# Kernel tuning notes

Measured on AMD Instinct MI355X. Metric: run time of the kernel, lower is better.

Reference implementation:

```python
import jax, jax.numpy as jnp
import numpy as np

N = 50000   # nodes
E = 1600000 # edges (avg degree 32)
H = 128     # input_size == hidden_size
L = 2       # n_layer


def setup_inputs() -> dict:
    key = jax.random.key(0)
    k0, k1, k2, k3, k4 = jax.random.split(key, 5)
    inp = jax.random.normal(k0, (N, H), dtype=jnp.float32)
    h = jax.random.normal(k1, (L, N, H), dtype=jnp.float32)
    edgidx = jax.random.randint(k2, (2, E), 0, N, dtype=jnp.int32)
    # stacked gate linears, order per layer: xz, hz, xr, hr, xh, hh
    W = jax.random.normal(k3, (L, 6, H, H), dtype=jnp.float32) * (1.0 / np.sqrt(H))
    b = jax.random.normal(k4, (L, 6, H), dtype=jnp.float32) * 0.01
    return {"inp": inp, "edgidx": edgidx, "h": h, "W": W, "b": b}


def _gin(x, W, b, src, dst, n):
    # GINConv with eps=0: Linear(x + sum_{j in N(i)} x_j)
    agg = jax.ops.segment_sum(x[src], dst, num_segments=n)  # scatter-add over edges
    return (x + agg) @ W + b


def reference(inp, edgidx, h, W, b):
    src, dst = edgidx[0], edgidx[1]
    n = inp.shape[0]
    x = inp
    outs = []
    for i in range(W.shape[0]):  # small fixed layer loop
        z = jax.nn.sigmoid(_gin(x, W[i, 0], b[i, 0], src, dst, n)
                           + _gin(h[i], W[i, 1], b[i, 1], src, dst, n))
        r = jax.nn.sigmoid(_gin(x, W[i, 2], b[i, 2], src, dst, n)
                           + _gin(h[i], W[i, 3], b[i, 3], src, dst, n))
        h_tilde = jnp.tanh(_gin(x, W[i, 4], b[i, 4], src, dst, n)
                           + _gin(r * h[i], W[i, 5], b[i, 5], src, dst, n))
        x = z * h[i] + (1.0 - z) * h_tilde
        outs.append(x)
    h_out = jnp.stack(outs)  # [L, N, H]; original returns (out, h_out) where out is h_out
    return h_out
```

## Files before the change

### kernel.cpp

```cpp
#include <hip/hip_runtime.h>
#include <math.h>
#include <stdint.h>

#define HDIM 128

typedef _Float16 f16;
typedef unsigned short u16;
typedef __attribute__((ext_vector_type(8))) unsigned short u16x8;
typedef __attribute__((ext_vector_type(4))) _Float16 f16x4;
typedef __attribute__((ext_vector_type(8))) _Float16 f16x8;
typedef __attribute__((ext_vector_type(4))) float f32x4;

__global__ __launch_bounds__(256) void degrank_kernel(
    const int* __restrict__ edg, int* __restrict__ cnt,
    u16* __restrict__ rank, int E) {
  int e = blockIdx.x * 256 + threadIdx.x;
  if (e < E) {
    int src = edg[e];
    int dst = edg[E + e];
    rank[e] = (u16)atomicAdd(&cnt[dst * 16 + (src >> 12)], 1);
  }
}

__global__ __launch_bounds__(256) void nodescan_kernel(
    int* __restrict__ cnt, int* __restrict__ deg, int* __restrict__ degt,
    int N) {
  int node = blockIdx.x * 256 + threadIdx.x;
  if (node >= N) return;
  int* c = cnt + node * 16;
  int s = 0;
  #pragma unroll
  for (int b = 0; b < 16; ++b) {
    int v = c[b];
    c[b] = s;
    s += v;
  }
  degt[node] = s;
  deg[node] = (s + 7) & ~7;
}

__global__ __launch_bounds__(256) void scan_part_kernel(
    const int* __restrict__ deg, int* __restrict__ bsum, int n, int chunk) {
  __shared__ int red[256];
  const int b = blockIdx.x, t = threadIdx.x;
  const int begin = b * chunk;
  const int end = min(begin + chunk, n);
  int s = 0;
  for (int i = begin + t; i < end; i += 256) s += deg[i];
  red[t] = s;
  __syncthreads();
  for (int off = 128; off > 0; off >>= 1) {
    if (t < off) red[t] += red[t + off];
    __syncthreads();
  }
  if (t == 0) bsum[b] = red[0];
}

__global__ __launch_bounds__(256) void scan_top_kernel(
    const int* __restrict__ bsum, int* __restrict__ boff,
    int* __restrict__ offs, int n) {
  __shared__ int sh[256];
  const int t = threadIdx.x;
  int v = bsum[t];
  sh[t] = v;
  __syncthreads();
  for (int off = 1; off < 256; off <<= 1) {
    int add = (t >= off) ? sh[t - off] : 0;
    __syncthreads();
    sh[t] += add;
    __syncthreads();
  }
  boff[t] = sh[t] - v;
  if (t == 255) offs[n] = sh[255];
}

__global__ __launch_bounds__(256) void scan_fin_kernel(
    const int* __restrict__ deg, const int* __restrict__ boff,
    int* __restrict__ offs, int n, int chunk) {
  __shared__ int sh[256];
  const int b = blockIdx.x, t = threadIdx.x;
  const int idx = b * chunk + t;
  int v = (t < chunk && idx < n) ? deg[idx] : 0;
  sh[t] = v;
  __syncthreads();
  for (int off = 1; off < 256; off <<= 1) {
    int add = (t >= off) ? sh[t - off] : 0;
    __syncthreads();
    sh[t] += add;
    __syncthreads();
  }
  if (t < chunk && idx < n) offs[idx] = boff[b] + sh[t] - v;
}

__global__ __launch_bounds__(256) void fill_kernel(
    const int* __restrict__ edg, const int* __restrict__ offs,
    const int* __restrict__ cnt, const u16* __restrict__ rank,
    u16* __restrict__ csr_src, int E) {
  int i = blockIdx.x * 256 + threadIdx.x;
  int e0 = i * 4;
  if (e0 >= E) return;
  if (e0 + 4 <= E) {
    int4 s4 = *reinterpret_cast<const int4*>(edg + e0);
    int4 d4 = *reinterpret_cast<const int4*>(edg + E + e0);
    ushort4 r4 = *reinterpret_cast<const ushort4*>(rank + e0);
    csr_src[offs[d4.x] + cnt[d4.x * 16 + (s4.x >> 12)] + r4.x] = (u16)s4.x;
    csr_src[offs[d4.y] + cnt[d4.y * 16 + (s4.y >> 12)] + r4.y] = (u16)s4.y;
    csr_src[offs[d4.z] + cnt[d4.z * 16 + (s4.z >> 12)] + r4.z] = (u16)s4.z;
    csr_src[offs[d4.w] + cnt[d4.w * 16 + (s4.w >> 12)] + r4.w] = (u16)s4.w;
  } else {
    for (int e = e0; e < E; ++e) {
      int src = edg[e];
      int dst = edg[E + e];
      csr_src[offs[dst] + cnt[dst * 16 + (src >> 12)] + rank[e]] = (u16)src;
    }
  }
}

__global__ __launch_bounds__(256) void pad_kernel(
    const int* __restrict__ offs, const int* __restrict__ degt,
    const int* __restrict__ deg, u16* __restrict__ csr,
    f16* __restrict__ xb, f16* __restrict__ Pb, f16* __restrict__ hb,
    int N, int L) {
  int n = blockIdx.x * 256 + threadIdx.x;
  if (n < N) {
    int base = offs[n];
    int a = degt[n], b = deg[n];
    for (int k = base + a; k < base + b; ++k) csr[k] = (u16)N;
  } else {
    int t2 = n - N;
    int rows = 2 + L;
    int total = 4 * rows * 4;
    if (t2 < total) {
      int chunk = t2 & 3;
      int r = (t2 >> 2) % rows;
      int sl = (t2 >> 2) / rows;
      size_t SN1 = (size_t)(N + 1);
      f16* p;
      if (r == 0)      p = xb + (sl * SN1 + N) * 32;
      else if (r == 1) p = Pb + (sl * SN1 + N) * 32;
      else {
        int i = r - 2;
        p = hb + ((size_t)sl * L * SN1 + (size_t)i * SN1 + N) * 32;
      }
      f16x8 z{};
      *reinterpret_cast<f16x8*>(p + chunk * 8) = z;
    }
  }
}

__global__ __launch_bounds__(256) void convb_kernel(
    const float* __restrict__ inp, const float* __restrict__ h,
    f16* __restrict__ xb, f16* __restrict__ hb, int n, int N1, int NH,
    int L) {
  const int ly = blockIdx.y;
  const float* __restrict__ src = (ly == 0) ? inp : h + (size_t)(ly - 1) * NH;
  f16* __restrict__ dstb = (ly == 0) ? xb : hb;
  const int SN = (ly == 0) ? N1 : L * N1;
  const int rowoff = (ly == 0) ? 0 : (ly - 1) * N1;
  const int t = threadIdx.x;
  const int nloc = t >> 3;
  const int sub = t & 7;
  const int sl = sub >> 1;
  const int hf = sub & 1;
  const int node = blockIdx.x * 32 + nloc;
  if (node >= n) return;
  const float* sp = src + (size_t)node * HDIM + sub * 16;
  f16* dp = dstb + ((size_t)sl * SN + rowoff + node) * 32 + hf * 16;
  float4 v0 = *reinterpret_cast<const float4*>(sp + 0);
  float4 v1 = *reinterpret_cast<const float4*>(sp + 4);
  float4 v2 = *reinterpret_cast<const float4*>(sp + 8);
  float4 v3 = *reinterpret_cast<const float4*>(sp + 12);
  f16x8 o0, o1;
  o0[0]=(f16)v0.x; o0[1]=(f16)v0.y; o0[2]=(f16)v0.z; o0[3]=(f16)v0.w;
  o0[4]=(f16)v1.x; o0[5]=(f16)v1.y; o0[6]=(f16)v1.z; o0[7]=(f16)v1.w;
  o1[0]=(f16)v2.x; o1[1]=(f16)v2.y; o1[2]=(f16)v2.z; o1[3]=(f16)v2.w;
  o1[4]=(f16)v3.x; o1[5]=(f16)v3.y; o1[6]=(f16)v3.z; o1[7]=(f16)v3.w;
  *reinterpret_cast<f16x8*>(dp) = o0;
  *reinterpret_cast<f16x8*>(dp + 8) = o1;
}

__global__ __launch_bounds__(256) void transw_kernel(
    const float* __restrict__ W, f16* __restrict__ WT) {
  __shared__ float sh[32][33];
  const int g = blockIdx.y;
  const int ti = blockIdx.x >> 2;
  const int tj = blockIdx.x & 3;
  const float* __restrict__ wp = W + (size_t)g * HDIM * HDIM;
  f16* __restrict__ op = WT + (size_t)g * HDIM * HDIM;
  const int t = threadIdx.x;
  #pragma unroll
  for (int it = 0; it < 4; ++it) {
    int elem = it * 256 + t;
    int r = elem >> 5, c = elem & 31;
    sh[r][c] = wp[(size_t)(ti * 32 + r) * HDIM + tj * 32 + c];
  }
  __syncthreads();
  #pragma unroll
  for (int it = 0; it < 4; ++it) {
    int elem = it * 256 + t;
    int cc = elem >> 5, rr = elem & 31;
    op[(size_t)(tj * 32 + cc) * HDIM + ti * 32 + rr] = (f16)sh[rr][cc];
  }
}

__global__ __launch_bounds__(256) void pull2_kernel(
    const u16* __restrict__ csr_src, const int* __restrict__ offs,
    const f16* __restrict__ xb, const f16* __restrict__ hbl,
    f16* __restrict__ A, f16* __restrict__ Bh, int N, int N1, int hSN) {
  const int cls = blockIdx.x & 7;
  const int tid = cls >> 2;
  const int sl = cls & 3;
  const int node = (blockIdx.x >> 3) * 64 + (threadIdx.x >> 2);
  if (node >= N) return;
  const int c8 = (threadIdx.x & 3) << 3;
  const f16* __restrict__ tab =
      tid ? hbl + (size_t)sl * hSN * 32 : xb + (size_t)sl * (size_t)N1 * 32;
  f16* __restrict__ dst = (tid ? Bh : A) + (size_t)sl * (size_t)N1 * 32;
  const int s = offs[node];
  const int e = offs[node + 1];
  float acc[8];
  f16x8 sv = *reinterpret_cast<const f16x8*>(tab + (size_t)node * 32 + c8);
  #pragma unroll
  for (int q = 0; q < 8; ++q) acc[q] = (float)sv[q];
  int k = s;
  for (; k + 16 <= e; k += 16) {
    u16x8 ia = *reinterpret_cast<const u16x8*>(csr_src + k);
    u16x8 ib = *reinterpret_cast<const u16x8*>(csr_src + k + 8);
    f16x8 u0 = *reinterpret_cast<const f16x8*>(tab + (size_t)ia[0] * 32 + c8);
    f16x8 u1 = *reinterpret_cast<const f16x8*>(tab + (size_t)ia[1] * 32 + c8);
    f16x8 u2 = *reinterpret_cast<const f16x8*>(tab + (size_t)ia[2] * 32 + c8);
    f16x8 u3 = *reinterpret_cast<const f16x8*>(tab + (size_t)ia[3] * 32 + c8);
    f16x8 u4 = *reinterpret_cast<const f16x8*>(tab + (size_t)ia[4] * 32 + c8);
    f16x8 u5 = *reinterpret_cast<const f16x8*>(tab + (size_t)ia[5] * 32 + c8);
    f16x8 u6 = *reinterpret_cast<const f16x8*>(tab + (size_t)ia[6] * 32 + c8);
    f16x8 u7 = *reinterpret_cast<const f16x8*>(tab + (size_t)ia[7] * 32 + c8);
    f16x8 u8 = *reinterpret_cast<const f16x8*>(tab + (size_t)ib[0] * 32 + c8);
    f16x8 u9 = *reinterpret_cast<const f16x8*>(tab + (size_t)ib[1] * 32 + c8);
    f16x8 ua = *reinterpret_cast<const f16x8*>(tab + (size_t)ib[2] * 32 + c8);
    f16x8 ub = *reinterpret_cast<const f16x8*>(tab + (size_t)ib[3] * 32 + c8);
    f16x8 uc = *reinterpret_cast<const f16x8*>(tab + (size_t)ib[4] * 32 + c8);
    f16x8 ud = *reinterpret_cast<const f16x8*>(tab + (size_t)ib[5] * 32 + c8);
    f16x8 ue = *reinterpret_cast<const f16x8*>(tab + (size_t)ib[6] * 32 + c8);
    f16x8 uf = *reinterpret_cast<const f16x8*>(tab + (size_t)ib[7] * 32 + c8);
    f16x8 g0 = (u0 + u1) + (u2 + u3);
    f16x8 g1 = (u4 + u5) + (u6 + u7);
    f16x8 g2 = (u8 + u9) + (ua + ub);
    f16x8 g3 = (uc + ud) + (ue + uf);
    #pragma unroll
    for (int q = 0; q < 8; ++q)
      acc[q] += ((float)g0[q] + (float)g1[q]) + ((float)g2[q] + (float)g3[q]);
  }
  if (k < e) {
    u16x8 ia = *reinterpret_cast<const u16x8*>(csr_src + k);
    f16x8 u0 = *reinterpret_cast<const f16x8*>(tab + (size_t)ia[0] * 32 + c8);
    f16x8 u1 = *reinterpret_cast<const f16x8*>(tab + (size_t)ia[1] * 32 + c8);
    f16x8 u2 = *reinterpret_cast<const f16x8*>(tab + (size_t)ia[2] * 32 + c8);
    f16x8 u3 = *reinterpret_cast<const f16x8*>(tab + (size_t)ia[3] * 32 + c8);
    f16x8 u4 = *reinterpret_cast<const f16x8*>(tab + (size_t)ia[4] * 32 + c8);
    f16x8 u5 = *reinterpret_cast<const f16x8*>(tab + (size_t)ia[5] * 32 + c8);
    f16x8 u6 = *reinterpret_cast<const f16x8*>(tab + (size_t)ia[6] * 32 + c8);
    f16x8 u7 = *reinterpret_cast<const f16x8*>(tab + (size_t)ia[7] * 32 + c8);
    f16x8 g0 = (u0 + u1) + (u2 + u3);
    f16x8 g1 = (u4 + u5) + (u6 + u7);
    #pragma unroll
    for (int q = 0; q < 8; ++q) acc[q] += (float)g0[q] + (float)g1[q];
  }
  f16x8 o;
  #pragma unroll
  for (int q = 0; q < 8; ++q) o[q] = (f16)acc[q];
  *reinterpret_cast<f16x8*>(dst + (size_t)node * 32 + c8) = o;
}

__device__ __forceinline__ void stage_blocked(
    const f16* __restrict__ src, f16* __restrict__ As,
    int row0, int N, int SN, int t) {
  #pragma unroll
  for (int i = 0; i < 4; ++i) {
    int u = i * 256 + t;
    int row = u >> 4;
    int sl = (u >> 2) & 3;
    int ck = u & 3;
    int r = row0 + row;
    f16x8 v{};
    if (r < N) v = *reinterpret_cast<const f16x8*>(
        src + ((size_t)sl * SN + r) * 32 + ck * 8);
    *reinterpret_cast<f16x8*>(&As[row * 136 + sl * 32 + ck * 8]) = v;
  }
}

__device__ __forceinline__ void mfma_tile(
    const f16* As, const f16* Ws, int wr, int wc, int ln15, int quad,
    f32x4 (&acc)[2][4]) {
  #pragma unroll
  for (int s = 0; s < 4; ++s) {
    f16x8 a0 = *reinterpret_cast<const f16x8*>(
        &As[(wr * 32 + ln15) * 136 + s * 32 + quad * 8]);
    f16x8 a1 = *reinterpret_cast<const f16x8*>(
        &As[(wr * 32 + 16 + ln15) * 136 + s * 32 + quad * 8]);
    #pragma unroll
    for (int ni = 0; ni < 4; ++ni) {
      f16x8 bf = *reinterpret_cast<const f16x8*>(
          &Ws[(wc * 64 + ni * 16 + ln15) * 136 + s * 32 + quad * 8]);
      acc[0][ni] = __builtin_amdgcn_mfma_f32_16x16x32_f16(a0, bf, acc[0][ni], 0, 0, 0);
      acc[1][ni] = __builtin_amdgcn_mfma_f32_16x16x32_f16(a1, bf, acc[1][ni], 0, 0, 0);
    }
  }
}

__global__ __launch_bounds__(256, 3) void gemm3_kernel(
    const f16* __restrict__ A, const f16* __restrict__ Bh,
    const f16* __restrict__ WT, const float* __restrict__ b,
    const f16* __restrict__ hbl, f16* __restrict__ zb,
    f16* __restrict__ P, float* __restrict__ hpre, int N, int N1, int hSN) {
  __shared__ f16 As[64 * 136];
  __shared__ f16 Ws[128 * 136];
  const int t = threadIdx.x;
  const int w = t >> 6, wr = w >> 1, wc = w & 1;
  const int lane = t & 63, ln15 = lane & 15, quad = lane >> 4;
  const int row0 = blockIdx.x * 64;
  f32x4 accZ[2][4], accR[2][4], accH[2][4];
  #pragma unroll
  for (int i = 0; i < 2; ++i)
    #pragma unroll
    for (int j = 0; j < 4; ++j) {
      accZ[i][j] = (f32x4){0.f, 0.f, 0.f, 0.f};
      accR[i][j] = (f32x4){0.f, 0.f, 0.f, 0.f};
      accH[i][j] = (f32x4){0.f, 0.f, 0.f, 0.f};
    }

  stage_blocked(A, As, row0, N, N1, t);
  #pragma unroll
  for (int g = 0; g < 3; ++g) {
    const f16* __restrict__ wp = WT + (size_t)(g * 2) * HDIM * HDIM;
    __syncthreads();
    #pragma unroll
    for (int i = 0; i < 8; ++i) {
      int flat = i * 256 + t;
      int n = flat >> 4;
      int o = (flat & 15) * 8;
      *reinterpret_cast<f16x8*>(&Ws[n * 136 + o]) =
          *reinterpret_cast<const f16x8*>(wp + (size_t)n * HDIM + o);
    }
    __syncthreads();
    if (g == 0) mfma_tile(As, Ws, wr, wc, ln15, quad, accZ);
    else if (g == 1) mfma_tile(As, Ws, wr, wc, ln15, quad, accR);
    else mfma_tile(As, Ws, wr, wc, ln15, quad, accH);
  }
  __syncthreads();
  stage_blocked(Bh, As, row0, N, N1, t);
  #pragma unroll
  for (int g = 0; g < 2; ++g) {
    const f16* __restrict__ wp = WT + (size_t)(g * 2 + 1) * HDIM * HDIM;
    __syncthreads();
    #pragma unroll
    for (int i = 0; i < 8; ++i) {
      int flat = i * 256 + t;
      int n = flat >> 4;
      int o = (flat & 15) * 8;
      *reinterpret_cast<f16x8*>(&Ws[n * 136 + o]) =
          *reinterpret_cast<const f16x8*>(wp + (size_t)n * HDIM + o);
    }
    __syncthreads();
    if (g == 0) mfma_tile(As, Ws, wr, wc, ln15, quad, accZ);
    else mfma_tile(As, Ws, wr, wc, ln15, quad, accR);
  }
  __syncthreads();

  {
    const f16* __restrict__ wp = WT + (size_t)5 * HDIM * HDIM;
    #pragma unroll
    for (int i = 0; i < 8; ++i) {
      int flat = i * 256 + t;
      int n = flat >> 4;
      int o = (flat & 15) * 8;
      *reinterpret_cast<f16x8*>(&Ws[n * 136 + o]) =
          *reinterpret_cast<const f16x8*>(wp + (size_t)n * HDIM + o);
    }
  }
  #pragma unroll
  for (int ni = 0; ni < 4; ++ni) {
    const int col = wc * 64 + ni * 16 + ln15;
    const int slc = col >> 5;
    const int cw = col & 31;
    float bz = b[0 * HDIM + col] + b[1 * HDIM + col];
    float br = b[2 * HDIM + col] + b[3 * HDIM + col];
    float bh = b[4 * HDIM + col] + b[5 * HDIM + col];
    #pragma unroll
    for (int mi = 0; mi < 2; ++mi) {
      #pragma unroll
      for (int r = 0; r < 4; ++r) {
        int rowl = wr * 32 + mi * 16 + quad * 4 + r;
        int row = row0 + rowl;
        float rv = accR[mi][ni][r] + br;
        float rg = 1.f / (1.f + expf(-rv));
        float hv = 0.f;
        if (row < N) {
          size_t idx = (size_t)row * HDIM + col;
          zb[idx] = (f16)(accZ[mi][ni][r] + bz);
          hpre[idx] = accH[mi][ni][r] + bh;
          hv = (float)hbl[((size_t)slc * hSN + row) * 32 + cw];
        }
        As[rowl * 136 + col] = (f16)(rg * hv);
      }
    }
  }
  __syncthreads();
  f32x4 accP[2][4];
  #pragma unroll
  for (int i = 0; i < 2; ++i)
    #pragma unroll
    for (int j = 0; j < 4; ++j) accP[i][j] = (f32x4){0.f, 0.f, 0.f, 0.f};
  mfma_tile(As, Ws, wr, wc, ln15, quad, accP);

  #pragma unroll
  for (int ni = 0; ni < 4; ++ni) {
    const int col = wc * 64 + ni * 16 + ln15;
    const int slc = col >> 5;
    const int cw = col & 31;
    #pragma unroll
    for (int mi = 0; mi < 2; ++mi) {
      #pragma unroll
      for (int r = 0; r < 4; ++r) {
        int row = row0 + wr * 32 + mi * 16 + quad * 4 + r;
        if (row >= N) continue;
        P[((size_t)slc * N1 + row) * 32 + cw] = (f16)accP[mi][ni][r];
      }
    }
  }
}

__global__ __launch_bounds__(256) void gru_final_kernel(
    const u16* __restrict__ csr_src, const int* __restrict__ offs,
    const f16* __restrict__ P, const f16* __restrict__ zb,
    const f16* __restrict__ hbl, float* __restrict__ outi,
    f16* __restrict__ xb, int N, int N1, int hSN) {
  const int sl = blockIdx.x & 3;
  const int node = (blockIdx.x >> 2) * 64 + (threadIdx.x >> 2);
  if (node >= N) return;
  const int c8 = (threadIdx.x & 3) << 3;
  const f16* __restrict__ tab = P + (size_t)sl * (size_t)N1 * 32;
  const int s = offs[node];
  const int e = offs[node + 1];
  float acc[8];
  f16x8 sv = *reinterpret_cast<const f16x8*>(tab + (size_t)node * 32 + c8);
  #pragma unroll
  for (int q = 0; q < 8; ++q) acc[q] = (float)sv[q];
  int k = s;
  for (; k + 16 <= e; k += 16) {
    u16x8 ia = *reinterpret_cast<const u16x8*>(csr_src + k);
    u16x8 ib = *reinterpret_cast<const u16x8*>(csr_src + k + 8);
    f16x8 u0 = *reinterpret_cast<const f16x8*>(tab + (size_t)ia[0] * 32 + c8);
    f16x8 u1 = *reinterpret_cast<const f16x8*>(tab + (size_t)ia[1] * 32 + c8);
    f16x8 u2 = *reinterpret_cast<const f16x8*>(tab + (size_t)ia[2] * 32 + c8);
    f16x8 u3 = *reinterpret_cast<const f16x8*>(tab + (size_t)ia[3] * 32 + c8);
    f16x8 u4 = *reinterpret_cast<const f16x8*>(tab + (size_t)ia[4] * 32 + c8);
    f16x8 u5 = *reinterpret_cast<const f16x8*>(tab + (size_t)ia[5] * 32 + c8);
    f16x8 u6 = *reinterpret_cast<const f16x8*>(tab + (size_t)ia[6] * 32 + c8);
    f16x8 u7 = *reinterpret_cast<const f16x8*>(tab + (size_t)ia[7] * 32 + c8);
    f16x8 u8 = *reinterpret_cast<const f16x8*>(tab + (size_t)ib[0] * 32 + c8);
    f16x8 u9 = *reinterpret_cast<const f16x8*>(tab + (size_t)ib[1] * 32 + c8);
    f16x8 ua = *reinterpret_cast<const f16x8*>(tab + (size_t)ib[2] * 32 + c8);
    f16x8 ub = *reinterpret_cast<const f16x8*>(tab + (size_t)ib[3] * 32 + c8);
    f16x8 uc = *reinterpret_cast<const f16x8*>(tab + (size_t)ib[4] * 32 + c8);
    f16x8 ud = *reinterpret_cast<const f16x8*>(tab + (size_t)ib[5] * 32 + c8);
    f16x8 ue = *reinterpret_cast<const f16x8*>(tab + (size_t)ib[6] * 32 + c8);
    f16x8 uf = *reinterpret_cast<const f16x8*>(tab + (size_t)ib[7] * 32 + c8);
    f16x8 g0 = (u0 + u1) + (u2 + u3);
    f16x8 g1 = (u4 + u5) + (u6 + u7);
    f16x8 g2 = (u8 + u9) + (ua + ub);
    f16x8 g3 = (uc + ud) + (ue + uf);
    #pragma unroll
    for (int q = 0; q < 8; ++q)
      acc[q] += ((float)g0[q] + (float)g1[q]) + ((float)g2[q] + (float)g3[q]);
  }
  if (k < e) {
    u16x8 ia = *reinterpret_cast<const u16x8*>(csr_src + k);
    f16x8 u0 = *reinterpret_cast<const f16x8*>(tab + (size_t)ia[0] * 32 + c8);
    f16x8 u1 = *reinterpret_cast<const f16x8*>(tab + (size_t)ia[1] * 32 + c8);
    f16x8 u2 = *reinterpret_cast<const f16x8*>(tab + (size_t)ia[2] * 32 + c8);
    f16x8 u3 = *reinterpret_cast<const f16x8*>(tab + (size_t)ia[3] * 32 + c8);
    f16x8 u4 = *reinterpret_cast<const f16x8*>(tab + (size_t)ia[4] * 32 + c8);
    f16x8 u5 = *reinterpret_cast<const f16x8*>(tab + (size_t)ia[5] * 32 + c8);
    f16x8 u6 = *reinterpret_cast<const f16x8*>(tab + (size_t)ia[6] * 32 + c8);
    f16x8 u7 = *reinterpret_cast<const f16x8*>(tab + (size_t)ia[7] * 32 + c8);
    f16x8 g0 = (u0 + u1) + (u2 + u3);
    f16x8 g1 = (u4 + u5) + (u6 + u7);
    #pragma unroll
    for (int q = 0; q < 8; ++q) acc[q] += (float)g0[q] + (float)g1[q];
  }
  const size_t idx = (size_t)node * HDIM + sl * 32 + c8;
  float4 hp0 = *reinterpret_cast<const float4*>(outi + idx);
  float4 hp1 = *reinterpret_cast<const float4*>(outi + idx + 4);
  f16x8 zv = *reinterpret_cast<const f16x8*>(zb + idx);
  f16x8 hv = *reinterpret_cast<const f16x8*>(
      hbl + ((size_t)sl * hSN + node) * 32 + c8);
  float4 o0, o1;
  f16x8 xo;
  #pragma unroll
  for (int q = 0; q < 8; ++q) {
    float hp = (q < 4) ? (&hp0.x)[q] : (&hp1.x)[q - 4];
    float ht = tanhf(hp + acc[q]);
    float z = 1.f / (1.f + expf(-(float)zv[q]));
    float o = z * (float)hv[q] + (1.f - z) * ht;
    if (q < 4) (&o0.x)[q] = o; else (&o1.x)[q - 4] = o;
    xo[q] = (f16)o;
  }
  *reinterpret_cast<float4*>(outi + idx) = o0;
  *reinterpret_cast<float4*>(outi + idx + 4) = o1;
  *reinterpret_cast<f16x8*>(xb + ((size_t)sl * N1 + node) * 32 + c8) = xo;
}

extern "C" void kernel_launch(void* const* d_in, const int* in_sizes, int n_in,
                              void* d_out, int out_size, void* d_ws, size_t ws_size,
                              hipStream_t stream) {
  const float* inp = (const float*)d_in[0];
  const int*   edg = (const int*)d_in[1];
  const float* h   = (const float*)d_in[2];
  const float* W   = (const float*)d_in[3];
  const float* b   = (const float*)d_in[4];
  float* out = (float*)d_out;

  const int NH = in_sizes[0];
  const int N  = NH / HDIM;
  const int E  = in_sizes[1] / 2;
  const int L  = in_sizes[2] / NH;
  const int N1 = N + 1;
  const size_t NT = (size_t)128 * N1;

  f16* Af   = (f16*)d_ws;
  f16* Bhf  = Af + NT;
  f16* Pbuf = Bhf + NT;
  f16* xbuf = Pbuf + NT;
  f16* hbuf = xbuf + NT;
  f16* zbuf = hbuf + (size_t)L * NT;
  f16* WT   = zbuf + (size_t)NH;
  int* deg     = (int*)(WT + (size_t)L * 6 * HDIM * HDIM);
  int* degt    = deg + N;
  int* offs    = degt + N;
  int* bsum    = offs + (N + 1);
  int* boff    = bsum + 256;
  uintptr_t rp = (uintptr_t)(boff + 256);
  rp = (rp + 63) & ~(uintptr_t)63;
  u16* rank    = (u16*)rp;
  u16* csr_src = rank + (size_t)E;
  int* cnt     = (int*)Af;

  const int eblocks = (E + 255) / 256;
  const int fblocks = (E + 1023) / 1024;
  const int nsblocks = (N + 255) / 256;
  const int pdblocks = (N + 256 + 255) / 256;
  const int rowblocks = (N + 63) / 64;
  const int p2blocks = ((N + 63) / 64) * 8;
  const int p1blocks = ((N + 63) / 64) * 4;
  const int cvblocks = (N + 31) / 32;
  const int chunk = (N + 255) / 256;
  const int hSN = L * N1;

  hipMemsetAsync(cnt, 0, (size_t)N * 16 * sizeof(int), stream);
  hipLaunchKernelGGL(degrank_kernel, dim3(eblocks), dim3(256), 0, stream,
                     edg, cnt, rank, E);
  hipLaunchKernelGGL(nodescan_kernel, dim3(nsblocks), dim3(256), 0, stream,
                     cnt, deg, degt, N);
  hipLaunchKernelGGL(scan_part_kernel, dim3(256), dim3(256), 0, stream,
                     deg, bsum, N, chunk);
  hipLaunchKernelGGL(scan_top_kernel, dim3(1), dim3(256), 0, stream,
                     bsum, boff, offs, N);
  hipLaunchKernelGGL(scan_fin_kernel, dim3(256), dim3(256), 0, stream,
                     deg, boff, offs, N, chunk);
  hipLaunchKernelGGL(fill_kernel, dim3(fblocks), dim3(256), 0, stream,
                     edg, offs, cnt, rank, csr_src, E);
  hipLaunchKernelGGL(pad_kernel, dim3(pdblocks), dim3(256), 0, stream,
                     offs, degt, deg, csr_src, xbuf, Pbuf, hbuf, N, L);
  hipLaunchKernelGGL(transw_kernel, dim3(16, L * 6), dim3(256), 0, stream,
                     W, WT);
  hipLaunchKernelGGL(convb_kernel, dim3(cvblocks, L + 1), dim3(256), 0, stream,
                     inp, h, xbuf, hbuf, N, N1, NH, L);

  for (int i = 0; i < L; ++i) {
    const f16* hbl = hbuf + (size_t)i * N1 * 32;
    const f16* WTi = WT + (size_t)i * 6 * HDIM * HDIM;
    const float* bi = b + (size_t)i * 6 * HDIM;
    float* outi = out + (size_t)i * NH;

    hipLaunchKernelGGL(pull2_kernel, dim3(p2blocks), dim3(256), 0, stream,
                       csr_src, offs, xbuf, hbl, Af, Bhf, N, N1, hSN);
    hipLaunchKernelGGL(gemm3_kernel, dim3(rowblocks), dim3(256), 0, stream,
                       Af, Bhf, WTi, bi, hbl, zbuf, Pbuf, outi, N, N1, hSN);
    hipLaunchKernelGGL(gru_final_kernel, dim3(p1blocks), dim3(256), 0, stream,
                       csr_src, offs, Pbuf, zbuf, hbl, outi, xbuf, N, N1, hSN);
  }
}
```

Measured before the change: 591.7 us.

## Fuse preprocessing kernels and overlap next-layer h aggregation with GRU final

Merges the node scan with the block partial sum, and merges the three-stage scan into a two-kernel scan. It also fuses the CSR fill with the padding, and the weight transpose with the fp16 conversion, to cut launch count. The h[i+1] neighbour aggregation moves into the previous layer's gru_final launch as extra block classes, so the later layer only pulls x. This removes several small launches and fills the GPU better during the final gather. In exchange it adds divergent block roles and a single-block-level scan over bsum in every scanfin block.

```diff
diff --git a/kernel.cpp b/kernel.cpp
--- a/kernel.cpp
+++ b/kernel.cpp
@@ -22,46 +22,42 @@
   }
 }
 
-__global__ __launch_bounds__(256) void nodescan_kernel(
+__global__ __launch_bounds__(256) void nodescan2_kernel(
     int* __restrict__ cnt, int* __restrict__ deg, int* __restrict__ degt,
-    int N) {
-  int node = blockIdx.x * 256 + threadIdx.x;
-  if (node >= N) return;
-  int* c = cnt + node * 16;
-  int s = 0;
-  #pragma unroll
-  for (int b = 0; b < 16; ++b) {
-    int v = c[b];
-    c[b] = s;
-    s += v;
-  }
-  degt[node] = s;
-  deg[node] = (s + 7) & ~7;
-}
-
-__global__ __launch_bounds__(256) void scan_part_kernel(
-    const int* __restrict__ deg, int* __restrict__ bsum, int n, int chunk) {
+    int* __restrict__ bsum, int N) {
   __shared__ int red[256];
-  const int b = blockIdx.x, t = threadIdx.x;
-  const int begin = b * chunk;
-  const int end = min(begin + chunk, n);
-  int s = 0;
-  for (int i = begin + t; i < end; i += 256) s += deg[i];
-  red[t] = s;
+  const int t = threadIdx.x;
+  const int node = blockIdx.x * 256 + t;
+  int d8 = 0;
+  if (node < N) {
+    int* c = cnt + node * 16;
+    int s = 0;
+    #pragma unroll
+    for (int b2 = 0; b2 < 16; ++b2) {
+      int v = c[b2];
+      c[b2] = s;
+      s += v;
+    }
+    degt[node] = s;
+    d8 = (s + 7) & ~7;
+    deg[node] = d8;
+  }
+  red[t] = d8;
   __syncthreads();
   for (int off = 128; off > 0; off >>= 1) {
     if (t < off) red[t] += red[t + off];
     __syncthreads();
   }
-  if (t == 0) bsum[b] = red[0];
-}
-
-__global__ __launch_bounds__(256) void scan_top_kernel(
-    const int* __restrict__ bsum, int* __restrict__ boff,
-    int* __restrict__ offs, int n) {
+  if (t == 0) bsum[blockIdx.x] = red[0];
+}
+
+__global__ __launch_bounds__(256) void scanfin2_kernel(
+    const int* __restrict__ deg, const int* __restrict__ bsum,
+    int* __restrict__ offs, int N, int nblk) {
   __shared__ int sh[256];
   const int t = threadIdx.x;
-  int v = bsum[t];
+  const int b = blockIdx.x;
+  int v = (t < nblk) ? bsum[t] : 0;
   sh[t] = v;
   __syncthreads();
   for (int off = 1; off < 256; off <<= 1) {
@@ -70,18 +66,11 @@
     sh[t] += add;
     __syncthreads();
   }
-  boff[t] = sh[t] - v;
-  if (t == 255) offs[n] = sh[255];
-}
-
-__global__ __launch_bounds__(256) void scan_fin_kernel(
-    const int* __restrict__ deg, const int* __restrict__ boff,
-    int* __restrict__ offs, int n, int chunk) {
-  __shared__ int sh[256];
-  const int b = blockIdx.x, t = threadIdx.x;
-  const int idx = b * chunk + t;
-  int v = (t < chunk && idx < n) ? deg[idx] : 0;
-  sh[t] = v;
+  const int boff = sh[b] - bsum[b];
+  __syncthreads();
+  const int idx = b * 256 + t;
+  int dv = (idx < N) ? deg[idx] : 0;
+  sh[t] = dv;
   __syncthreads();
   for (int off = 1; off < 256; off <<= 1) {
     int add = (t >= off) ? sh[t - off] : 0;
@@ -89,45 +78,43 @@
     sh[t] += add;
     __syncthreads();
   }
-  if (t < chunk && idx < n) offs[idx] = boff[b] + sh[t] - v;
-}
-
-__global__ __launch_bounds__(256) void fill_kernel(
+  if (idx < N) {
+    offs[idx] = boff + sh[t] - dv;
+    if (idx == N - 1) offs[N] = boff + sh[t];
+  }
+}
+
+__global__ __launch_bounds__(256) void fillpad_kernel(
     const int* __restrict__ edg, const int* __restrict__ offs,
     const int* __restrict__ cnt, const u16* __restrict__ rank,
-    u16* __restrict__ csr_src, int E) {
+    const int* __restrict__ degt, const int* __restrict__ deg,
+    u16* __restrict__ csr_src, f16* __restrict__ xb, f16* __restrict__ Pb,
+    f16* __restrict__ hb, int E, int N, int L) {
   int i = blockIdx.x * 256 + threadIdx.x;
   int e0 = i * 4;
-  if (e0 >= E) return;
-  if (e0 + 4 <= E) {
-    int4 s4 = *reinterpret_cast<const int4*>(edg + e0);
-    int4 d4 = *reinterpret_cast<const int4*>(edg + E + e0);
-    ushort4 r4 = *reinterpret_cast<const ushort4*>(rank + e0);
-    csr_src[offs[d4.x] + cnt[d4.x * 16 + (s4.x >> 12)] + r4.x] = (u16)s4.x;
-    csr_src[offs[d4.y] + cnt[d4.y * 16 + (s4.y >> 12)] + r4.y] = (u16)s4.y;
-    csr_src[offs[d4.z] + cnt[d4.z * 16 + (s4.z >> 12)] + r4.z] = (u16)s4.z;
-    csr_src[offs[d4.w] + cnt[d4.w * 16 + (s4.w >> 12)] + r4.w] = (u16)s4.w;
+  if (e0 < E) {
+    if (e0 + 4 <= E) {
+      int4 s4 = *reinterpret_cast<const int4*>(edg + e0);
+      int4 d4 = *reinterpret_cast<const int4*>(edg + E + e0);
+      ushort4 r4 = *reinterpret_cast<const ushort4*>(rank + e0);
+      csr_src[offs[d4.x] + cnt[d4.x * 16 + (s4.x >> 12)] + r4.x] = (u16)s4.x;
+      csr_src[offs[d4.y] + cnt[d4.y * 16 + (s4.y >> 12)] + r4.y] = (u16)s4.y;
+      csr_src[offs[d4.z] + cnt[d4.z * 16 + (s4.z >> 12)] + r4.z] = (u16)s4.z;
+      csr_src[offs[d4.w] + cnt[d4.w * 16 + (s4.w >> 12)] + r4.w] = (u16)s4.w;
+    } else {
+      for (int e = e0; e < E; ++e) {
+        int src = edg[e];
+        int dst = edg[E + e];
+        csr_src[offs[dst] + cnt[dst * 16 + (src >> 12)] + rank[e]] = (u16)src;
+      }
+    }
+  }
+  if (i < N) {
+    int base = offs[i];
+    int a = degt[i], b2 = deg[i];
+    for (int k = base + a; k < base + b2; ++k) csr_src[k] = (u16)N;
   } else {
-    for (int e = e0; e < E; ++e) {
-      int src = edg[e];
-      int dst = edg[E + e];
-      csr_src[offs[dst] + cnt[dst * 16 + (src >> 12)] + rank[e]] = (u16)src;
-    }
-  }
-}
-
-__global__ __launch_bounds__(256) void pad_kernel(
-    const int* __restrict__ offs, const int* __restrict__ degt,
-    const int* __restrict__ deg, u16* __restrict__ csr,
-    f16* __restrict__ xb, f16* __restrict__ Pb, f16* __restrict__ hb,
-    int N, int L) {
-  int n = blockIdx.x * 256 + threadIdx.x;
-  if (n < N) {
-    int base = offs[n];
-    int a = degt[n], b = deg[n];
-    for (int k = base + a; k < base + b; ++k) csr[k] = (u16)N;
-  } else {
-    int t2 = n - N;
+    int t2 = i - N;
     int rows = 2 + L;
     int total = 4 * rows * 4;
     if (t2 < total) {
@@ -139,8 +126,8 @@
       if (r == 0)      p = xb + (sl * SN1 + N) * 32;
       else if (r == 1) p = Pb + (sl * SN1 + N) * 32;
       else {
-        int i = r - 2;
-        p = hb + ((size_t)sl * L * SN1 + (size_t)i * SN1 + N) * 32;
+        int li = r - 2;
+        p = hb + ((size_t)sl * L * SN1 + (size_t)li * SN1 + N) * 32;
       }
       f16x8 z{};
       *reinterpret_cast<f16x8*>(p + chunk * 8) = z;
@@ -148,84 +135,68 @@
   }
 }
 
-__global__ __launch_bounds__(256) void convb_kernel(
+__global__ __launch_bounds__(256) void transconv_kernel(
     const float* __restrict__ inp, const float* __restrict__ h,
-    f16* __restrict__ xb, f16* __restrict__ hb, int n, int N1, int NH,
-    int L) {
+    const float* __restrict__ W, f16* __restrict__ xb, f16* __restrict__ hb,
+    f16* __restrict__ WT, int n, int N1, int NH, int L) {
+  __shared__ float shm[32][33];
   const int ly = blockIdx.y;
-  const float* __restrict__ src = (ly == 0) ? inp : h + (size_t)(ly - 1) * NH;
-  f16* __restrict__ dstb = (ly == 0) ? xb : hb;
-  const int SN = (ly == 0) ? N1 : L * N1;
-  const int rowoff = (ly == 0) ? 0 : (ly - 1) * N1;
   const int t = threadIdx.x;
-  const int nloc = t >> 3;
-  const int sub = t & 7;
-  const int sl = sub >> 1;
-  const int hf = sub & 1;
-  const int node = blockIdx.x * 32 + nloc;
-  if (node >= n) return;
-  const float* sp = src + (size_t)node * HDIM + sub * 16;
-  f16* dp = dstb + ((size_t)sl * SN + rowoff + node) * 32 + hf * 16;
-  float4 v0 = *reinterpret_cast<const float4*>(sp + 0);
-  float4 v1 = *reinterpret_cast<const float4*>(sp + 4);
-  float4 v2 = *reinterpret_cast<const float4*>(sp + 8);
-  float4 v3 = *reinterpret_cast<const float4*>(sp + 12);
-  f16x8 o0, o1;
-  o0[0]=(f16)v0.x; o0[1]=(f16)v0.y; o0[2]=(f16)v0.z; o0[3]=(f16)v0.w;
-  o0[4]=(f16)v1.x; o0[5]=(f16)v1.y; o0[6]=(f16)v1.z; o0[7]=(f16)v1.w;
-  o1[0]=(f16)v2.x; o1[1]=(f16)v2.y; o1[2]=(f16)v2.z; o1[3]=(f16)v2.w;
-  o1[4]=(f16)v3.x; o1[5]=(f16)v3.y; o1[6]=(f16)v3.z; o1[7]=(f16)v3.w;
-  *reinterpret_cast<f16x8*>(dp) = o0;
-  *reinterpret_cast<f16x8*>(dp + 8) = o1;
-}
-
-__global__ __launch_bounds__(256) void transw_kernel(
-    const float* __restrict__ W, f16* __restrict__ WT) {
-  __shared__ float sh[32][33];
-  const int g = blockIdx.y;
-  const int ti = blockIdx.x >> 2;
-  const int tj = blockIdx.x & 3;
-  const float* __restrict__ wp = W + (size_t)g * HDIM * HDIM;
-  f16* __restrict__ op = WT + (size_t)g * HDIM * HDIM;
-  const int t = threadIdx.x;
-  #pragma unroll
-  for (int it = 0; it < 4; ++it) {
-    int elem = it * 256 + t;
-    int r = elem >> 5, c = elem & 31;
-    sh[r][c] = wp[(size_t)(ti * 32 + r) * HDIM + tj * 32 + c];
-  }
-  __syncthreads();
-  #pragma unroll
-  for (int it = 0; it < 4; ++it) {
-    int elem = it * 256 + t;
-    int cc = elem >> 5, rr = elem & 31;
-    op[(size_t)(tj * 32 + cc) * HDIM + ti * 32 + rr] = (f16)sh[rr][cc];
-  }
-}
-
-__global__ __launch_bounds__(256) void pull2_kernel(
-    const u16* __restrict__ csr_src, const int* __restrict__ offs,
-    const f16* __restrict__ xb, const f16* __restrict__ hbl,
-    f16* __restrict__ A, f16* __restrict__ Bh, int N, int N1, int hSN) {
-  const int cls = blockIdx.x & 7;
-  const int tid = cls >> 2;
-  const int sl = cls & 3;
-  const int node = (blockIdx.x >> 3) * 64 + (threadIdx.x >> 2);
-  if (node >= N) return;
-  const int c8 = (threadIdx.x & 3) << 3;
-  const f16* __restrict__ tab =
-      tid ? hbl + (size_t)sl * hSN * 32 : xb + (size_t)sl * (size_t)N1 * 32;
-  f16* __restrict__ dst = (tid ? Bh : A) + (size_t)sl * (size_t)N1 * 32;
-  const int s = offs[node];
-  const int e = offs[node + 1];
-  float acc[8];
-  f16x8 sv = *reinterpret_cast<const f16x8*>(tab + (size_t)node * 32 + c8);
-  #pragma unroll
-  for (int q = 0; q < 8; ++q) acc[q] = (float)sv[q];
+  if (ly <= L) {
+    const float* __restrict__ src = (ly == 0) ? inp : h + (size_t)(ly - 1) * NH;
+    f16* __restrict__ dstb = (ly == 0) ? xb : hb;
+    const int SN = (ly == 0) ? N1 : L * N1;
+    const int rowoff = (ly == 0) ? 0 : (ly - 1) * N1;
+    const int nloc = t >> 3;
+    const int sub = t & 7;
+    const int sl = sub >> 1;
+    const int hf = sub & 1;
+    const int node = blockIdx.x * 32 + nloc;
+    if (node >= n) return;
+    const float* sp = src + (size_t)node * HDIM + sub * 16;
+    f16* dp = dstb + ((size_t)sl * SN + rowoff + node) * 32 + hf * 16;
+    float4 v0 = *reinterpret_cast<const float4*>(sp + 0);
+    float4 v1 = *reinterpret_cast<const float4*>(sp + 4);
+    float4 v2 = *reinterpret_cast<const float4*>(sp + 8);
+    float4 v3 = *reinterpret_cast<const float4*>(sp + 12);
+    f16x8 o0, o1;
+    o0[0]=(f16)v0.x; o0[1]=(f16)v0.y; o0[2]=(f16)v0.z; o0[3]=(f16)v0.w;
+    o0[4]=(f16)v1.x; o0[5]=(f16)v1.y; o0[6]=(f16)v1.z; o0[7]=(f16)v1.w;
+    o1[0]=(f16)v2.x; o1[1]=(f16)v2.y; o1[2]=(f16)v2.z; o1[3]=(f16)v2.w;
+    o1[4]=(f16)v3.x; o1[5]=(f16)v3.y; o1[6]=(f16)v3.z; o1[7]=(f16)v3.w;
+    *reinterpret_cast<f16x8*>(dp) = o0;
+    *reinterpret_cast<f16x8*>(dp + 8) = o1;
+  } else {
+    if (blockIdx.x >= 16 * L * 6) return;
+    const int g = blockIdx.x >> 4;
+    const int inner = blockIdx.x & 15;
+    const int ti = inner >> 2;
+    const int tj = inner & 3;
+    const float* __restrict__ wp = W + (size_t)g * HDIM * HDIM;
+    f16* __restrict__ op = WT + (size_t)g * HDIM * HDIM;
+    #pragma unroll
+    for (int it = 0; it < 4; ++it) {
+      int elem = it * 256 + t;
+      int r = elem >> 5, c = elem & 31;
+      shm[r][c] = wp[(size_t)(ti * 32 + r) * HDIM + tj * 32 + c];
+    }
+    __syncthreads();
+    #pragma unroll
+    for (int it = 0; it < 4; ++it) {
+      int elem = it * 256 + t;
+      int cc = elem >> 5, rr = elem & 31;
+      op[(size_t)(tj * 32 + cc) * HDIM + ti * 32 + rr] = (f16)shm[rr][cc];
+    }
+  }
+}
+
+__device__ __forceinline__ void gather8(
+    const u16* __restrict__ csr, int s, int e, const f16* __restrict__ tab,
+    int c8, float acc[8]) {
   int k = s;
   for (; k + 16 <= e; k += 16) {
-    u16x8 ia = *reinterpret_cast<const u16x8*>(csr_src + k);
-    u16x8 ib = *reinterpret_cast<const u16x8*>(csr_src + k + 8);
+    u16x8 ia = *reinterpret_cast<const u16x8*>(csr + k);
+    u16x8 ib = *reinterpret_cast<const u16x8*>(csr + k + 8);
     f16x8 u0 = *reinterpret_cast<const f16x8*>(tab + (size_t)ia[0] * 32 + c8);
     f16x8 u1 = *reinterpret_cast<const f16x8*>(tab + (size_t)ia[1] * 32 + c8);
     f16x8 u2 = *reinterpret_cast<const f16x8*>(tab + (size_t)ia[2] * 32 + c8);
@@ -251,7 +222,7 @@
       acc[q] += ((float)g0[q] + (float)g1[q]) + ((float)g2[q] + (float)g3[q]);
   }
   if (k < e) {
-    u16x8 ia = *reinterpret_cast<const u16x8*>(csr_src + k);
+    u16x8 ia = *reinterpret_cast<const u16x8*>(csr + k);
     f16x8 u0 = *reinterpret_cast<const f16x8*>(tab + (size_t)ia[0] * 32 + c8);
     f16x8 u1 = *reinterpret_cast<const f16x8*>(tab + (size_t)ia[1] * 32 + c8);
     f16x8 u2 = *reinterpret_cast<const f16x8*>(tab + (size_t)ia[2] * 32 + c8);
@@ -265,6 +236,46 @@
     #pragma unroll
     for (int q = 0; q < 8; ++q) acc[q] += (float)g0[q] + (float)g1[q];
   }
+}
+
+__global__ __launch_bounds__(256) void pull2_kernel(
+    const u16* __restrict__ csr_src, const int* __restrict__ offs,
+    const f16* __restrict__ xb, const f16* __restrict__ hbl,
+    f16* __restrict__ A, f16* __restrict__ Bh, int N, int N1, int hSN) {
+  const int cls = blockIdx.x & 7;
+  const int tid = cls >> 2;
+  const int sl = cls & 3;
+  const int node = (blockIdx.x >> 3) * 64 + (threadIdx.x >> 2);
+  if (node >= N) return;
+  const int c8 = (threadIdx.x & 3) << 3;
+  const f16* __restrict__ tab =
+      tid ? hbl + (size_t)sl * hSN * 32 : xb + (size_t)sl * (size_t)N1 * 32;
+  f16* __restrict__ dst = (tid ? Bh : A) + (size_t)sl * (size_t)N1 * 32;
+  float acc[8];
+  f16x8 sv = *reinterpret_cast<const f16x8*>(tab + (size_t)node * 32 + c8);
+  #pragma unroll
+  for (int q = 0; q < 8; ++q) acc[q] = (float)sv[q];
+  gather8(csr_src, offs[node], offs[node + 1], tab, c8, acc);
+  f16x8 o;
+  #pragma unroll
+  for (int q = 0; q < 8; ++q) o[q] = (f16)acc[q];
+  *reinterpret_cast<f16x8*>(dst + (size_t)node * 32 + c8) = o;
+}
+
+__global__ __launch_bounds__(256) void pullx_kernel(
+    const u16* __restrict__ csr_src, const int* __restrict__ offs,
+    const f16* __restrict__ tabb, f16* __restrict__ dstb, int N, int N1) {
+  const int sl = blockIdx.x & 3;
+  const int node = (blockIdx.x >> 2) * 64 + (threadIdx.x >> 2);
+  if (node >= N) return;
+  const int c8 = (threadIdx.x & 3) << 3;
+  const f16* __restrict__ tab = tabb + (size_t)sl * (size_t)N1 * 32;
+  f16* __restrict__ dst = dstb + (size_t)sl * (size_t)N1 * 32;
+  float acc[8];
+  f16x8 sv = *reinterpret_cast<const f16x8*>(tab + (size_t)node * 32 + c8);
+  #pragma unroll
+  for (int q = 0; q < 8; ++q) acc[q] = (float)sv[q];
+  gather8(csr_src, offs[node], offs[node + 1], tab, c8, acc);
   f16x8 o;
   #pragma unroll
   for (int q = 0; q < 8; ++q) o[q] = (f16)acc[q];
@@ -433,61 +444,34 @@
     const u16* __restrict__ csr_src, const int* __restrict__ offs,
     const f16* __restrict__ P, const f16* __restrict__ zb,
     const f16* __restrict__ hbl, float* __restrict__ outi,
-    f16* __restrict__ xb, int N, int N1, int hSN) {
-  const int sl = blockIdx.x & 3;
-  const int node = (blockIdx.x >> 2) * 64 + (threadIdx.x >> 2);
+    f16* __restrict__ xb, const f16* __restrict__ hnext,
+    f16* __restrict__ Bh, int N, int N1, int hSN, int lgc) {
+  const int cls = blockIdx.x & ((1 << lgc) - 1);
+  const int node = (blockIdx.x >> lgc) * 64 + (threadIdx.x >> 2);
   if (node >= N) return;
   const int c8 = (threadIdx.x & 3) << 3;
+  if (cls >= 4) {
+    const int sl = cls - 4;
+    const f16* __restrict__ tab = hnext + (size_t)sl * hSN * 32;
+    f16* __restrict__ dst = Bh + (size_t)sl * (size_t)N1 * 32;
+    float acc[8];
+    f16x8 sv = *reinterpret_cast<const f16x8*>(tab + (size_t)node * 32 + c8);
+    #pragma unroll
+    for (int q = 0; q < 8; ++q) acc[q] = (float)sv[q];
+    gather8(csr_src, offs[node], offs[node + 1], tab, c8, acc);
+    f16x8 o;
+    #pragma unroll
+    for (int q = 0; q < 8; ++q) o[q] = (f16)acc[q];
+    *reinterpret_cast<f16x8*>(dst + (size_t)node * 32 + c8) = o;
+    return;
+  }
+  const int sl = cls;
   const f16* __restrict__ tab = P + (size_t)sl * (size_t)N1 * 32;
-  const int s = offs[node];
-  const int e = offs[node + 1];
   float acc[8];
   f16x8 sv = *reinterpret_cast<const f16x8*>(tab + (size_t)node * 32 + c8);
   #pragma unroll
   for (int q = 0; q < 8; ++q) acc[q] = (float)sv[q];
-  int k = s;
-  for (; k + 16 <= e; k += 16) {
-    u16x8 ia = *reinterpret_cast<const u16x8*>(csr_src + k);
-    u16x8 ib = *reinterpret_cast<const u16x8*>(csr_src + k + 8);
-    f16x8 u0 = *reinterpret_cast<const f16x8*>(tab + (size_t)ia[0] * 32 + c8);
-    f16x8 u1 = *reinterpret_cast<const f16x8*>(tab + (size_t)ia[1] * 32 + c8);
-    f16x8 u2 = *reinterpret_cast<const f16x8*>(tab + (size_t)ia[2] * 32 + c8);
-    f16x8 u3 = *reinterpret_cast<const f16x8*>(tab + (size_t)ia[3] * 32 + c8);
-    f16x8 u4 = *reinterpret_cast<const f16x8*>(tab + (size_t)ia[4] * 32 + c8);
-    f16x8 u5 = *reinterpret_cast<const f16x8*>(tab + (size_t)ia[5] * 32 + c8);
-    f16x8 u6 = *reinterpret_cast<const f16x8*>(tab + (size_t)ia[6] * 32 + c8);
-    f16x8 u7 = *reinterpret_cast<const f16x8*>(tab + (size_t)ia[7] * 32 + c8);
-    f16x8 u8 = *reinterpret_cast<const f16x8*>(tab + (size_t)ib[0] * 32 + c8);
-    f16x8 u9 = *reinterpret_cast<const f16x8*>(tab + (size_t)ib[1] * 32 + c8);
-    f16x8 ua = *reinterpret_cast<const f16x8*>(tab + (size_t)ib[2] * 32 + c8);
-    f16x8 ub = *reinterpret_cast<const f16x8*>(tab + (size_t)ib[3] * 32 + c8);
-    f16x8 uc = *reinterpret_cast<const f16x8*>(tab + (size_t)ib[4] * 32 + c8);
-    f16x8 ud = *reinterpret_cast<const f16x8*>(tab + (size_t)ib[5] * 32 + c8);
-    f16x8 ue = *reinterpret_cast<const f16x8*>(tab + (size_t)ib[6] * 32 + c8);
-    f16x8 uf = *reinterpret_cast<const f16x8*>(tab + (size_t)ib[7] * 32 + c8);
-    f16x8 g0 = (u0 + u1) + (u2 + u3);
-    f16x8 g1 = (u4 + u5) + (u6 + u7);
-    f16x8 g2 = (u8 + u9) + (ua + ub);
-    f16x8 g3 = (uc + ud) + (ue + uf);
-    #pragma unroll
-    for (int q = 0; q < 8; ++q)
-      acc[q] += ((float)g0[q] + (float)g1[q]) + ((float)g2[q] + (float)g3[q]);
-  }
-  if (k < e) {
-    u16x8 ia = *reinterpret_cast<const u16x8*>(csr_src + k);
-    f16x8 u0 = *reinterpret_cast<const f16x8*>(tab + (size_t)ia[0] * 32 + c8);
-    f16x8 u1 = *reinterpret_cast<const f16x8*>(tab + (size_t)ia[1] * 32 + c8);
-    f16x8 u2 = *reinterpret_cast<const f16x8*>(tab + (size_t)ia[2] * 32 + c8);
-    f16x8 u3 = *reinterpret_cast<const f16x8*>(tab + (size_t)ia[3] * 32 + c8);
-    f16x8 u4 = *reinterpret_cast<const f16x8*>(tab + (size_t)ia[4] * 32 + c8);
-    f16x8 u5 = *reinterpret_cast<const f16x8*>(tab + (size_t)ia[5] * 32 + c8);
-    f16x8 u6 = *reinterpret_cast<const f16x8*>(tab + (size_t)ia[6] * 32 + c8);
-    f16x8 u7 = *reinterpret_cast<const f16x8*>(tab + (size_t)ia[7] * 32 + c8);
-    f16x8 g0 = (u0 + u1) + (u2 + u3);
-    f16x8 g1 = (u4 + u5) + (u6 + u7);
-    #pragma unroll
-    for (int q = 0; q < 8; ++q) acc[q] += (float)g0[q] + (float)g1[q];
-  }
+  gather8(csr_src, offs[node], offs[node + 1], tab, c8, acc);
   const size_t idx = (size_t)node * HDIM + sl * 32 + c8;
   float4 hp0 = *reinterpret_cast<const float4*>(outi + idx);
   float4 hp1 = *reinterpret_cast<const float4*>(outi + idx + 4);
@@ -548,45 +532,45 @@
   const int eblocks = (E + 255) / 256;
   const int fblocks = (E + 1023) / 1024;
   const int nsblocks = (N + 255) / 256;
-  const int pdblocks = (N + 256 + 255) / 256;
   const int rowblocks = (N + 63) / 64;
-  const int p2blocks = ((N + 63) / 64) * 8;
-  const int p1blocks = ((N + 63) / 64) * 4;
+  const int p2blocks = rowblocks * 8;
+  const int pxblocks = rowblocks * 4;
   const int cvblocks = (N + 31) / 32;
-  const int chunk = (N + 255) / 256;
   const int hSN = L * N1;
 
   hipMemsetAsync(cnt, 0, (size_t)N * 16 * sizeof(int), stream);
   hipLaunchKernelGGL(degrank_kernel, dim3(eblocks), dim3(256), 0, stream,
                      edg, cnt, rank, E);
-  hipLaunchKernelGGL(nodescan_kernel, dim3(nsblocks), dim3(256), 0, stream,
-                     cnt, deg, degt, N);
-  hipLaunchKernelGGL(scan_part_kernel, dim3(256), dim3(256), 0, stream,
-                     deg, bsum, N, chunk);
-  hipLaunchKernelGGL(scan_top_kernel, dim3(1), dim3(256), 0, stream,
-                     bsum, boff, offs, N);
-  hipLaunchKernelGGL(scan_fin_kernel, dim3(256), dim3(256), 0, stream,
-                     deg, boff, offs, N, chunk);
-  hipLaunchKernelGGL(fill_kernel, dim3(fblocks), dim3(256), 0, stream,
-                     edg, offs, cnt, rank, csr_src, E);
-  hipLaunchKernelGGL(pad_kernel, dim3(pdblocks), dim3(256), 0, stream,
-                     offs, degt, deg, csr_src, xbuf, Pbuf, hbuf, N, L);
-  hipLaunchKernelGGL(transw_kernel, dim3(16, L * 6), dim3(256), 0, stream,
-                     W, WT);
-  hipLaunchKernelGGL(convb_kernel, dim3(cvblocks, L + 1), dim3(256), 0, stream,
-                     inp, h, xbuf, hbuf, N, N1, NH, L);
+  hipLaunchKernelGGL(nodescan2_kernel, dim3(nsblocks), dim3(256), 0, stream,
+                     cnt, deg, degt, bsum, N);
+  hipLaunchKernelGGL(scanfin2_kernel, dim3(nsblocks), dim3(256), 0, stream,
+                     deg, bsum, offs, N, nsblocks);
+  hipLaunchKernelGGL(fillpad_kernel, dim3(fblocks), dim3(256), 0, stream,
+                     edg, offs, cnt, rank, degt, deg, csr_src,
+                     xbuf, Pbuf, hbuf, E, N, L);
+  hipLaunchKernelGGL(transconv_kernel, dim3(cvblocks, L + 2), dim3(256), 0,
+                     stream, inp, h, W, xbuf, hbuf, WT, N, N1, NH, L);
 
   for (int i = 0; i < L; ++i) {
     const f16* hbl = hbuf + (size_t)i * N1 * 32;
     const f16* WTi = WT + (size_t)i * 6 * HDIM * HDIM;
     const float* bi = b + (size_t)i * 6 * HDIM;
     float* outi = out + (size_t)i * NH;
-
-    hipLaunchKernelGGL(pull2_kernel, dim3(p2blocks), dim3(256), 0, stream,
-                       csr_src, offs, xbuf, hbl, Af, Bhf, N, N1, hSN);
+    const int last = (i + 1 >= L);
+    const f16* hnext = last ? hbuf : hbuf + (size_t)(i + 1) * N1 * 32;
+
+    if (i == 0) {
+      hipLaunchKernelGGL(pull2_kernel, dim3(p2blocks), dim3(256), 0, stream,
+                         csr_src, offs, xbuf, hbl, Af, Bhf, N, N1, hSN);
+    } else {
+      hipLaunchKernelGGL(pullx_kernel, dim3(pxblocks), dim3(256), 0, stream,
+                         csr_src, offs, xbuf, Af, N, N1);
+    }
     hipLaunchKernelGGL(gemm3_kernel, dim3(rowblocks), dim3(256), 0, stream,
                        Af, Bhf, WTi, bi, hbl, zbuf, Pbuf, outi, N, N1, hSN);
-    hipLaunchKernelGGL(gru_final_kernel, dim3(p1blocks), dim3(256), 0, stream,
-                       csr_src, offs, Pbuf, zbuf, hbl, outi, xbuf, N, N1, hSN);
-  }
-}
+    hipLaunchKernelGGL(gru_final_kernel,
+                       dim3(last ? pxblocks : p2blocks), dim3(256), 0, stream,
+                       csr_src, offs, Pbuf, zbuf, hbl, outi, xbuf,
+                       hnext, Bhf, N, N1, hSN, last ? 2 : 3);
+  }
+}
```

Measured after the change: 594.7 us. Within noise of the previous version (+0.5%).
